# Optimization experiments

Measured on AMD Instinct MI355X. Metric: run time of the kernel, lower is better.

Reference implementation:

```python
import jax, jax.numpy as jnp
import numpy as np

B, N, N2 = 4, 4096, 4096
CIN, DIM, KNN, UP = 128, 64, 20, 2
HPOS, HATT = 64, 256
EPS = 1e-5


def _group(feat, idx):
    # feat: (B,C,M), idx: (B,N,K) -> (B,C,N,K) gather of neighbor features
    return jax.vmap(lambda f, i: f[:, i])(feat, idx)


def _conv1d(w, b, x):
    # 1x1 Conv1d: w (O,C), x (B,C,N)
    return jnp.einsum('oc,bcn->bon', w, x) + b[:, None]


def _bn(x, g, be, m, v):
    # eval-mode BatchNorm2d on (B,C,N,K)
    inv = g / jnp.sqrt(v + EPS)
    return x * inv[:, None, None] + (be - m * inv)[:, None, None]


def setup_inputs() -> dict:
    key = jax.random.key(0)
    ks = jax.random.split(key, 32)
    r = lambda i, s: jax.random.normal(ks[i], s, jnp.float32)
    u = lambda i, s: jax.random.uniform(ks[i], s, jnp.float32, 0.5, 1.5)
    return {
        'pos1': r(0, (B, 3, N)),
        'query': r(1, (B, CIN, N)),
        'pos2': r(2, (B, 3, N2)),
        'key_feat': r(3, (B, CIN, N2)),
        'wq': r(4, (DIM, CIN)) * 0.05, 'bq': r(5, (DIM,)) * 0.05,
        'wk': r(6, (DIM, CIN)) * 0.05, 'bk': r(7, (DIM,)) * 0.05,
        'wv': r(8, (DIM, CIN)) * 0.05, 'bv': r(9, (DIM,)) * 0.05,
        'pw1': r(10, (HPOS, 3)) * 0.2, 'pb1': r(11, (HPOS,)) * 0.05,
        'pg': u(12, (HPOS,)), 'pbt': r(13, (HPOS,)) * 0.05,
        'pm': r(14, (HPOS,)) * 0.05, 'pv': u(15, (HPOS,)),
        'pw2': r(16, (DIM, HPOS)) * 0.1, 'pb2': r(17, (DIM,)) * 0.05,
        'aw1': r(18, (HATT, DIM)) * 0.1, 'ab1': r(19, (HATT,)) * 0.05,
        'ag': u(20, (HATT,)), 'abt2': r(21, (HATT,)) * 0.05,
        'am': r(22, (HATT,)) * 0.05, 'av': u(23, (HATT,)),
        'awt': r(24, (HATT, DIM, UP)) * 0.05, 'abt': r(25, (DIM,)) * 0.05,
        'we': r(26, (CIN, DIM)) * 0.1, 'be': r(27, (CIN,)) * 0.05,
    }


def reference(pos1, query, pos2, key_feat, wq, bq, wk, bk, wv, bv,
              pw1, pb1, pg, pbt, pm, pv, pw2, pb2,
              aw1, ab1, ag, abt2, am, av, awt, abt, we, be):
    q = _conv1d(wq, bq, query)          # (B,DIM,N)
    k = _conv1d(wk, bk, key_feat)       # (B,DIM,N2)
    v = _conv1d(wv, bv, key_feat)       # (B,DIM,N2)
    # KNN of pos1 queries into pos2 support set
    p1 = pos1.transpose(0, 2, 1)        # (B,N,3)
    p2 = pos2.transpose(0, 2, 1)        # (B,N2,3)
    d = (jnp.sum(p1 * p1, -1)[:, :, None] + jnp.sum(p2 * p2, -1)[:, None, :]
         - 2.0 * jnp.einsum('bnd,bmd->bnm', p1, p2))
    _, idx = jax.lax.top_k(-d, KNN)     # (B,N,KNN)
    kg = _group(k, idx)                 # (B,DIM,N,K)
    qk_rel = q[:, :, :, None] - kg
    pos_rel = pos1[:, :, :, None] - _group(pos2, idx)   # (B,3,N,K)
    # pos_mlp: conv2d 3->HPOS, BN, ReLU, conv2d HPOS->DIM
    pe = jnp.einsum('oc,bcnk->bonk', pw1, pos_rel) + pb1[:, None, None]
    pe = jax.nn.relu(_bn(pe, pg, pbt, pm, pv))
    pe = jnp.einsum('oc,bcnk->bonk', pw2, pe) + pb2[:, None, None]  # (B,DIM,N,K)
    # attn_mlp: conv2d DIM->HATT, BN, ReLU, ConvTranspose2d HATT->DIM kernel (UP,1)
    h = qk_rel + pe
    a = jnp.einsum('oc,bcnk->bonk', aw1, h) + ab1[:, None, None]
    a = jax.nn.relu(_bn(a, ag, abt2, am, av))               # (B,HATT,N,K)
    att = jnp.einsum('bcnk,cor->bonrk', a, awt).reshape(B, DIM, N * UP, KNN)
    att = att + abt[:, None, None]
    att = jax.nn.softmax(att, axis=-1)
    vg = _group(v, idx) + pe            # (B,DIM,N,K)
    vu = jnp.repeat(vg, UP, axis=2)     # nearest upsample -> (B,DIM,N*UP,K)
    agg = jnp.sum(att * vu, axis=-1)    # (B,DIM,N*UP)
    y = _conv1d(we, be, agg)            # (B,CIN,N*UP)
    identity = jnp.repeat(query, UP, axis=2)  # residual (in==out -> Identity)
    return y + identity
```

## Files before the change

### kernel.cpp

```cpp
#include <hip/hip_runtime.h>
#include <hip/hip_bf16.h>

#define BATCH 4
#define NPTS  4096
#define NPTS2 4096
#define CIN   128
#define DIM   64
#define KNN   20
#define UPF   2
#define HPOS  64
#define HATT  256
#define MOUT  8192
#define EPSF  1e-5f
#define QPB   3
#define BPB   1366

typedef _Float16 h16x8 __attribute__((ext_vector_type(8)));
typedef _Float16 h16x4 __attribute__((ext_vector_type(4)));
typedef _Float16 h16x2 __attribute__((ext_vector_type(2)));
typedef float    f32x4 __attribute__((ext_vector_type(4)));

__device__ inline float rdlane(float v, int src) {
  return __int_as_float(__builtin_amdgcn_readlane(__float_as_int(v), src));
}

__device__ __forceinline__ float distf(float qn, float m2x, float m2y, float m2z,
                                       float x, float y, float z) {
  float s = __fmaf_rn(x, x, qn);
  s = __fmaf_rn(y, y, s);
  s = __fmaf_rn(z, z, s);
  s = __fmaf_rn(m2x, x, s);
  s = __fmaf_rn(m2y, y, s);
  s = __fmaf_rn(m2z, z, s);
  return s;
}

__global__ __launch_bounds__(256) void proj_q(const float* __restrict__ x,
    const float* __restrict__ wq, const float* __restrict__ bq,
    float* __restrict__ q_t) {
  __shared__ float X[CIN][64];
  __shared__ float O[64][65];
  const int b  = blockIdx.x >> 6;
  const int n0 = (blockIdx.x & 63) * 64;
  const int t  = threadIdx.x;
  for (int l = t; l < CIN * 64; l += 256) {
    int c = l >> 6, i = l & 63;
    X[c][i] = x[(b * CIN + c) * NPTS + n0 + i];
  }
  __syncthreads();
  const int n_l = t & 63;
  const int w   = __builtin_amdgcn_readfirstlane(t >> 6);
  float acc[16];
#pragma unroll
  for (int i = 0; i < 16; ++i) acc[i] = bq[w * 16 + i];
  for (int c = 0; c < CIN; ++c) {
    float xv = X[c][n_l];
#pragma unroll
    for (int i = 0; i < 16; ++i) acc[i] += wq[(w * 16 + i) * CIN + c] * xv;
  }
#pragma unroll
  for (int i = 0; i < 16; ++i) O[n_l][w * 16 + i] = acc[i];
  __syncthreads();
  for (int l = t; l < 64 * 64; l += 256)
    q_t[(b * NPTS + n0 + (l >> 6)) * DIM + (l & 63)] = O[l >> 6][l & 63];
}

__global__ __launch_bounds__(256) void proj_kv(const float* __restrict__ x,
    const float* __restrict__ wk, const float* __restrict__ bk,
    const float* __restrict__ wv, const float* __restrict__ bv,
    float* __restrict__ k_t, float* __restrict__ v_t) {
  __shared__ float X[CIN][64];
  __shared__ float O[64][65];
  const int b  = blockIdx.x >> 6;
  const int n0 = (blockIdx.x & 63) * 64;
  const int t  = threadIdx.x;
  for (int l = t; l < CIN * 64; l += 256) {
    int c = l >> 6, i = l & 63;
    X[c][i] = x[(b * CIN + c) * NPTS2 + n0 + i];
  }
  __syncthreads();
  const int n_l = t & 63;
  const int w   = __builtin_amdgcn_readfirstlane(t >> 6);
  float acck[16], accv[16];
#pragma unroll
  for (int i = 0; i < 16; ++i) { acck[i] = bk[w * 16 + i]; accv[i] = bv[w * 16 + i]; }
  for (int c = 0; c < CIN; ++c) {
    float xv = X[c][n_l];
#pragma unroll
    for (int i = 0; i < 16; ++i) {
      acck[i] += wk[(w * 16 + i) * CIN + c] * xv;
      accv[i] += wv[(w * 16 + i) * CIN + c] * xv;
    }
  }
#pragma unroll
  for (int i = 0; i < 16; ++i) O[n_l][w * 16 + i] = acck[i];
  __syncthreads();
  for (int l = t; l < 64 * 64; l += 256)
    k_t[(b * NPTS2 + n0 + (l >> 6)) * DIM + (l & 63)] = O[l >> 6][l & 63];
  __syncthreads();
#pragma unroll
  for (int i = 0; i < 16; ++i) O[n_l][w * 16 + i] = accv[i];
  __syncthreads();
  for (int l = t; l < 64 * 64; l += 256)
    v_t[(b * NPTS2 + n0 + (l >> 6)) * DIM + (l & 63)] = O[l >> 6][l & 63];
}

__global__ __launch_bounds__(256) void knn_kernel(const float* __restrict__ pos1,
    const float* __restrict__ pos2, int* __restrict__ idxout) {
  __shared__ int   cntS[4];
  __shared__ float dbufS[4][64];
  __shared__ int   jbufS[4][64];
  const int lane = threadIdx.x & 63;
  const int wv   = threadIdx.x >> 6;
  const int g    = blockIdx.x * 4 + wv;
  const int b    = g >> 12;
  const int n    = g & (NPTS - 1);
  const float qx = pos1[(b * 3 + 0) * NPTS + n];
  const float qy = pos1[(b * 3 + 1) * NPTS + n];
  const float qz = pos1[(b * 3 + 2) * NPTS + n];
  const float qn = qx * qx + qy * qy + qz * qz;
  const float m2x = -2.0f * qx, m2y = -2.0f * qy, m2z = -2.0f * qz;
  const float* p2x = pos2 + (b * 3 + 0) * NPTS2;
  const float* p2y = pos2 + (b * 3 + 1) * NPTS2;
  const float* p2z = pos2 + (b * 3 + 2) * NPTS2;

  float mymin = 3.402823466e38f;
  for (int j0 = 0; j0 < NPTS2; j0 += 64) {
    int j = j0 + lane;
    float d = distf(qn, m2x, m2y, m2z, p2x[j], p2y[j], p2z[j]);
    mymin = fminf(mymin, d);
  }
  float v = mymin;
#pragma unroll
  for (int k = 2; k <= 64; k <<= 1) {
#pragma unroll
    for (int jj = k >> 1; jj >= 1; jj >>= 1) {
      float o = __shfl_xor(v, jj);
      bool up = ((lane & k) == 0);
      bool keepmin = (((lane & jj) == 0) == up);
      v = keepmin ? fminf(v, o) : fmaxf(v, o);
    }
  }
  const float T0 = rdlane(v, 19);

  if (lane == 0) cntS[wv] = 0;
  __syncthreads();

  for (int j0 = 0; j0 < NPTS2; j0 += 64) {
    int j = j0 + lane;
    float d = distf(qn, m2x, m2y, m2z, p2x[j], p2y[j], p2z[j]);
    if (d <= T0) {
      int slot = atomicAdd(&cntS[wv], 1);
      if (slot < 64) { dbufS[wv][slot] = d; jbufS[wv][slot] = j; }
    }
  }
  __syncthreads();

  const int cnt = cntS[wv];
  if (cnt <= 64) {
    float dk = (lane < cnt) ? dbufS[wv][lane] : 3.402823466e38f;
    int   jk = (lane < cnt) ? jbufS[wv][lane] : 0x7fffffff;
#pragma unroll
    for (int k = 2; k <= 64; k <<= 1) {
#pragma unroll
      for (int jj = k >> 1; jj >= 1; jj >>= 1) {
        float od = __shfl_xor(dk, jj);
        int   oj = __shfl_xor(jk, jj);
        bool mineSm = (dk < od) || (dk == od && jk < oj);
        bool up = ((lane & k) == 0);
        bool keepmin = (((lane & jj) == 0) == up);
        bool takeOther = (keepmin != mineSm);
        dk = takeOther ? od : dk;
        jk = takeOther ? oj : jk;
      }
    }
    if (lane < KNN) idxout[(b * NPTS + n) * KNN + lane] = jk;
  } else {
    float dl = 3.402823466e38f;
    int   il = 0;
    for (int j0 = 0; j0 < NPTS2; j0 += 64) {
      int j = j0 + lane;
      float d = distf(qn, m2x, m2y, m2z, p2x[j], p2y[j], p2z[j]);
      float T = rdlane(dl, 19);
      unsigned long long m = __ballot(d < T);
      while (m) {
        int src = __ffsll(m) - 1;
        m &= m - 1;
        float dd = rdlane(d, src);
        float T2 = rdlane(dl, 19);
        if (dd < T2) {
          int jj2 = j0 + src;
          float pd = __shfl_up(dl, 1);
          int   pi = __shfl_up(il, 1);
          if (dl > dd) {
            if (lane == 0 || pd <= dd) { dl = dd; il = jj2; }
            else                       { dl = pd; il = pi; }
          }
        }
      }
    }
    if (lane < KNN) idxout[(b * NPTS + n) * KNN + lane] = il;
  }
}

__global__ __launch_bounds__(256) void pack_weights(
    const float* __restrict__ aw1, const float* __restrict__ awt,
    const float* __restrict__ pw2,
    const float* __restrict__ ag,  const float* __restrict__ av,
    const float* __restrict__ abt2, const float* __restrict__ am,
    const float* __restrict__ abt,
    const float* __restrict__ pg,  const float* __restrict__ pv,
    const float* __restrict__ pbt, const float* __restrict__ pm,
    const float* __restrict__ ab1, const float* __restrict__ pb1,
    const float* __restrict__ pw1,
    _Float16* __restrict__ aw1h, _Float16* __restrict__ awtP,
    _Float16* __restrict__ pw2h, float* __restrict__ abtX,
    float* __restrict__ ab1f, float* __restrict__ pw1f,
    float* __restrict__ pb1f) {
  int i = blockIdx.x * 256 + threadIdx.x;
  if (i < 16384) {
    int j = i >> 6;
    float inv = ag[j] / sqrtf(av[j] + EPSF);
    aw1h[i] = (_Float16)(aw1[i] * inv);
  }
  if (i < 32768) {
    int orr = i >> 8, j = i & 255;
    awtP[i] = (_Float16)awt[j * 128 + orr];
  }
  if (i < 4096) pw2h[i] = (_Float16)pw2[i];
  if (i < 256) {
    float inv = ag[i] / sqrtf(av[i] + EPSF);
    ab1f[i] = ab1[i] * inv + (abt2[i] - am[i] * inv);
  }
  if (i < 192) {
    int hc = i / 3;
    float inv = pg[hc] / sqrtf(pv[hc] + EPSF);
    pw1f[i] = pw1[i] * inv;
  }
  if (i < 128) abtX[i] = abt[i >> 1];
  if (i < 64) {
    float inv = pg[i] / sqrtf(pv[i] + EPSF);
    pb1f[i] = pb1[i] * inv + (pbt[i] - pm[i] * inv);
  }
}

#define SM_H1B   0
#define SM_HB    0
#define SM_ALQ   0
#define SM_PEL   9216
#define SM_LGC   9216
#define SM_SJ    17920
#define SM_VGB   18176

__global__ __launch_bounds__(256, 4) void attn_mfma(
    const float* __restrict__ q_t, const float* __restrict__ k_t,
    const float* __restrict__ v_t, const int* __restrict__ idx,
    const float* __restrict__ pos1, const float* __restrict__ pos2,
    const float* __restrict__ pw1f, const float* __restrict__ pb1f,
    const _Float16* __restrict__ pw2h, const float* __restrict__ pb2,
    const _Float16* __restrict__ aw1h, const float* __restrict__ ab1f,
    const _Float16* __restrict__ awtP, const float* __restrict__ abtX,
    float* __restrict__ agg) {
  __shared__ __align__(16) char smem[26880];
  const int b  = blockIdx.x / BPB;
  const int n0 = (blockIdx.x - b * BPB) * QPB;
  const int t  = threadIdx.x;
  const int lane = t & 63;
  const int w  = t >> 6;
  const int r  = lane & 15;
  const int q4 = lane >> 4;

  int* sj = (int*)(smem + SM_SJ);

  if (t < 64) {
    int col = t;
    int p = col / 20, kk = col - p * 20;
    int nq = n0 + p;
    int vI = 0;
    if (p < QPB && nq < NPTS) vI = idx[(b * NPTS + nq) * KNN + kk];
    sj[col] = vI;
  }
  __syncthreads();

  const int colB = t & 63, cgB = t >> 6;
  const int pB = colB / 20;
  const bool okB = (pB < QPB) && (n0 + pB < NPTS);
  f32x4 qv4[4], kv4[4], vv4[4];
  {
    int jB  = sj[colB];
    int nqB = okB ? (n0 + pB) : 0;
    const float* qrow = q_t + ((size_t)(b * NPTS  + nqB)) * DIM + cgB * 16;
    const float* krow = k_t + ((size_t)(b * NPTS2 + jB))  * DIM + cgB * 16;
    const float* vrow = v_t + ((size_t)(b * NPTS2 + jB))  * DIM + cgB * 16;
#pragma unroll
    for (int u = 0; u < 4; ++u) {
      qv4[u] = *(const f32x4*)(qrow + u * 4);
      kv4[u] = *(const f32x4*)(krow + u * 4);
      vv4[u] = *(const f32x4*)(vrow + u * 4);
    }
  }

  {
    int col = t & 63, hg = t >> 6;
    int p = col / 20;
    int j = sj[col];
    bool okc = (p < QPB) && (n0 + p < NPTS);
    float p0 = 0.f, p1 = 0.f, p2 = 0.f;
    if (okc) {
      int nq = n0 + p;
      p0 = pos1[(b * 3 + 0) * NPTS + nq] - pos2[(b * 3 + 0) * NPTS2 + j];
      p1 = pos1[(b * 3 + 1) * NPTS + nq] - pos2[(b * 3 + 1) * NPTS2 + j];
      p2 = pos1[(b * 3 + 2) * NPTS + nq] - pos2[(b * 3 + 2) * NPTS2 + j];
    }
#pragma unroll
    for (int ii = 0; ii < 16; ii += 2) {
      int hc = hg * 16 + ii;
      float v0 = pb1f[hc]     + pw1f[hc*3]   * p0 + pw1f[hc*3+1] * p1 + pw1f[hc*3+2] * p2;
      float v1 = pb1f[hc + 1] + pw1f[hc*3+3] * p0 + pw1f[hc*3+4] * p1 + pw1f[hc*3+5] * p2;
      v0 = fmaxf(v0, 0.f);
      v1 = fmaxf(v1, 0.f);
      if (!okc) { v0 = 0.f; v1 = 0.f; }
      h16x2 pk = {(_Float16)v0, (_Float16)v1};
      *(h16x2*)(smem + SM_H1B + ((col * 72 + hc) * 2)) = pk;
    }
  }
  __syncthreads();

  {
    h16x8 a0[2];
#pragma unroll
    for (int ks = 0; ks < 2; ++ks)
      a0[ks] = *(const h16x8*)&pw2h[(w * 16 + r) * 64 + ks * 32 + q4 * 8];
    f32x4 acc[4];
#pragma unroll
    for (int nt = 0; nt < 4; ++nt) acc[nt] = (f32x4){0.f, 0.f, 0.f, 0.f};
#pragma unroll
    for (int ks = 0; ks < 2; ++ks)
#pragma unroll
      for (int nt = 0; nt < 4; ++nt) {
        h16x8 bv = *(h16x8*)(smem + SM_H1B + ((nt * 16 + r) * 72 + ks * 32 + q4 * 8) * 2);
        acc[nt] = __builtin_amdgcn_mfma_f32_16x16x32_f16(a0[ks], bv, acc[nt], 0, 0, 0);
      }
    int o0 = w * 16 + q4 * 4;
    f32x4 pbv = *(const f32x4*)&pb2[o0];
#pragma unroll
    for (int nt = 0; nt < 4; ++nt) {
      f32x4 vv = acc[nt] + pbv;
      h16x4 pk = {(_Float16)vv[0], (_Float16)vv[1], (_Float16)vv[2], (_Float16)vv[3]};
      *(h16x4*)(smem + SM_PEL + ((nt * 16 + r) * 68 + o0) * 2) = pk;
    }
  }
  __syncthreads();

  {
#pragma unroll
    for (int u = 0; u < 4; ++u) {
      int c0 = cgB * 16 + u * 4;
      h16x4 peh = *(h16x4*)(smem + SM_PEL + (colB * 68 + c0) * 2);
      f32x4 pe = {(float)peh[0], (float)peh[1], (float)peh[2], (float)peh[3]};
      f32x4 hv = qv4[u] - kv4[u] + pe;
      f32x4 gv = vv4[u] + pe;
      if (!okB) { hv = (f32x4){0.f,0.f,0.f,0.f}; gv = hv; }
      h16x4 hp = {(_Float16)hv[0], (_Float16)hv[1], (_Float16)hv[2], (_Float16)hv[3]};
      h16x4 gp = {(_Float16)gv[0], (_Float16)gv[1], (_Float16)gv[2], (_Float16)gv[3]};
      *(h16x4*)(smem + SM_HB  + (colB * 72 + c0) * 2) = hp;
      *(h16x4*)(smem + SM_VGB + (colB * 68 + c0) * 2) = gp;
    }
  }
  __syncthreads();

  h16x8 bs[2][4];
#pragma unroll
  for (int ks = 0; ks < 2; ++ks)
#pragma unroll
    for (int nt = 0; nt < 4; ++nt)
      bs[ks][nt] = *(h16x8*)(smem + SM_HB + ((nt * 16 + r) * 72 + ks * 32 + q4 * 8) * 2);
  __syncthreads();

  f32x4 accD[2][4];
#pragma unroll
  for (int h = 0; h < 2; ++h)
#pragma unroll
    for (int nt = 0; nt < 4; ++nt) accD[h][nt] = (f32x4){0.f, 0.f, 0.f, 0.f};

#pragma unroll
  for (int quar = 0; quar < 4; ++quar) {
    {
      int mt = quar * 4 + w;
      h16x8 af0 = *(const h16x8*)&aw1h[(mt * 16 + r) * 64 + q4 * 8];
      h16x8 af1 = *(const h16x8*)&aw1h[(mt * 16 + r) * 64 + 32 + q4 * 8];
      f32x4 acc[4];
#pragma unroll
      for (int nt = 0; nt < 4; ++nt) acc[nt] = (f32x4){0.f, 0.f, 0.f, 0.f};
#pragma unroll
      for (int nt = 0; nt < 4; ++nt)
        acc[nt] = __builtin_amdgcn_mfma_f32_16x16x32_f16(af0, bs[0][nt], acc[nt], 0, 0, 0);
#pragma unroll
      for (int nt = 0; nt < 4; ++nt)
        acc[nt] = __builtin_amdgcn_mfma_f32_16x16x32_f16(af1, bs[1][nt], acc[nt], 0, 0, 0);
      int j0  = mt * 16 + q4 * 4;
      int jq0 = j0 - quar * 64;
      f32x4 b1 = *(const f32x4*)&ab1f[j0];
#pragma unroll
      for (int nt = 0; nt < 4; ++nt) {
        int col = nt * 16 + r;
        float v0 = fmaxf(acc[nt][0] + b1[0], 0.f);
        float v1 = fmaxf(acc[nt][1] + b1[1], 0.f);
        float v2 = fmaxf(acc[nt][2] + b1[2], 0.f);
        float v3 = fmaxf(acc[nt][3] + b1[3], 0.f);
        h16x4 pk = {(_Float16)v0, (_Float16)v1, (_Float16)v2, (_Float16)v3};
        *(h16x4*)(smem + SM_ALQ + (col * 72 + jq0) * 2) = pk;
      }
    }
    __syncthreads();

#pragma unroll
    for (int ks2 = 0; ks2 < 2; ++ks2) {
      h16x8 bsv[4];
#pragma unroll
      for (int nt = 0; nt < 4; ++nt)
        bsv[nt] = *(h16x8*)(smem + SM_ALQ + ((nt * 16 + r) * 72 + ks2 * 32 + q4 * 8) * 2);
      int ksg = quar * 2 + ks2;
#pragma unroll
      for (int h = 0; h < 2; ++h) {
        int mt2 = w * 2 + h;
        h16x8 af = *(const h16x8*)&awtP[(mt2 * 16 + r) * 256 + ksg * 32 + q4 * 8];
#pragma unroll
        for (int nt = 0; nt < 4; ++nt)
          accD[h][nt] = __builtin_amdgcn_mfma_f32_16x16x32_f16(af, bsv[nt], accD[h][nt], 0, 0, 0);
      }
    }
    __syncthreads();
  }

  {
    const int li0 = w * 16 + q4 * 4;
#pragma unroll
    for (int h = 0; h < 2; ++h) {
      if (h) __syncthreads();
      int orr0 = (w * 2 + h) * 16 + q4 * 4;
      f32x4 ab = *(const f32x4*)&abtX[orr0];
#pragma unroll
      for (int nt = 0; nt < 4; ++nt) {
        int col = nt * 16 + r;
        if (col < QPB * KNN) {
          f32x4 vv = accD[h][nt] + ab;
          h16x4 pk = {(_Float16)vv[0], (_Float16)vv[1], (_Float16)vv[2], (_Float16)vv[3]};
          *(h16x4*)(smem + SM_LGC + (col * 68 + li0) * 2) = pk;
        }
      }
      __syncthreads();
      if (t < 64 * QPB) {
        int li = t & 63, p = t >> 6;
        if (n0 + p < NPTS) {
          int w2 = li >> 4;
          int orr = w2 * 32 + h * 16 + (li & 15);
          int o = orr >> 1, rb = orr & 1;
          float L[KNN];
#pragma unroll
          for (int kk = 0; kk < KNN; ++kk)
            L[kk] = (float)*(_Float16*)(smem + SM_LGC + (((p * 20 + kk) * 68 + li) * 2));
          float mx = L[0];
#pragma unroll
          for (int kk = 1; kk < KNN; ++kk) mx = fmaxf(mx, L[kk]);
          float s = 0.f;
#pragma unroll
          for (int kk = 0; kk < KNN; ++kk) { L[kk] = __expf(L[kk] - mx); s += L[kk]; }
          float rs = 1.0f / s;
          float a = 0.f;
#pragma unroll
          for (int kk = 0; kk < KNN; ++kk) {
            _Float16 gv = *(_Float16*)(smem + SM_VGB + (((p * 20 + kk) * 68 + o) * 2));
            a += L[kk] * (float)gv;
          }
          agg[(((size_t)(b * NPTS + n0 + p)) * UPF + rb) * DIM + o] = a * rs;
        }
      }
    }
  }
}

__global__ __launch_bounds__(256) void out_proj(const float* __restrict__ agg,
    const float* __restrict__ we, const float* __restrict__ be,
    const float* __restrict__ query, float* __restrict__ out) {
  __shared__ float A[64][65];
  const int b  = blockIdx.x >> 7;
  const int m0 = (blockIdx.x & 127) * 64;
  const int t  = threadIdx.x;
  for (int l = t; l < 64 * 64; l += 256) {
    int row = l >> 6, c = l & 63;
    A[row][c] = agg[(b * MOUT + m0 + row) * DIM + c];
  }
  __syncthreads();
  const int m_l = t & 63;
  const int w   = __builtin_amdgcn_readfirstlane(t >> 6);
  float acc[32];
#pragma unroll
  for (int i = 0; i < 32; ++i) acc[i] = 0.f;
  for (int c = 0; c < DIM; ++c) {
    float a = A[m_l][c];
#pragma unroll
    for (int i = 0; i < 32; ++i) acc[i] += we[(w * 32 + i) * DIM + c] * a;
  }
  const int m = m0 + m_l;
#pragma unroll
  for (int i = 0; i < 32; ++i) {
    int o = w * 32 + i;
    out[(b * CIN + o) * MOUT + m] = acc[i] + be[o] + query[(b * CIN + o) * NPTS + (m >> 1)];
  }
}

extern "C" void kernel_launch(void* const* d_in, const int* in_sizes, int n_in,
                              void* d_out, int out_size, void* d_ws, size_t ws_size,
                              hipStream_t stream) {
  (void)in_sizes; (void)n_in; (void)out_size; (void)ws_size;
  const float* pos1     = (const float*)d_in[0];
  const float* query    = (const float*)d_in[1];
  const float* pos2     = (const float*)d_in[2];
  const float* key_feat = (const float*)d_in[3];
  const float* wq  = (const float*)d_in[4];
  const float* bq  = (const float*)d_in[5];
  const float* wk  = (const float*)d_in[6];
  const float* bk  = (const float*)d_in[7];
  const float* wv  = (const float*)d_in[8];
  const float* bv  = (const float*)d_in[9];
  const float* pw1 = (const float*)d_in[10];
  const float* pb1 = (const float*)d_in[11];
  const float* pg  = (const float*)d_in[12];
  const float* pbt = (const float*)d_in[13];
  const float* pm  = (const float*)d_in[14];
  const float* pv  = (const float*)d_in[15];
  const float* pw2 = (const float*)d_in[16];
  const float* pb2 = (const float*)d_in[17];
  const float* aw1 = (const float*)d_in[18];
  const float* ab1 = (const float*)d_in[19];
  const float* ag  = (const float*)d_in[20];
  const float* abt2= (const float*)d_in[21];
  const float* am  = (const float*)d_in[22];
  const float* av  = (const float*)d_in[23];
  const float* awt = (const float*)d_in[24];
  const float* abt = (const float*)d_in[25];
  const float* we  = (const float*)d_in[26];
  const float* be  = (const float*)d_in[27];

  float* ws   = (float*)d_ws;
  float* q_t  = ws;
  float* k_t  = q_t + BATCH * NPTS * DIM;
  float* v_t  = k_t + BATCH * NPTS2 * DIM;
  float* aggb = v_t + BATCH * NPTS2 * DIM;
  int*   idxb = (int*)(aggb + BATCH * MOUT * DIM);
  _Float16* aw1h = (_Float16*)(idxb + BATCH * NPTS * KNN);
  _Float16* awtP = aw1h + HATT * DIM;
  _Float16* pw2h = awtP + 128 * HATT;
  float* abtX    = (float*)(pw2h + DIM * HPOS);
  float* ab1f    = abtX + 128;
  float* pw1f    = ab1f + HATT;
  float* pb1f    = pw1f + HPOS * 3;

  pack_weights<<<128, 256, 0, stream>>>(aw1, awt, pw2, ag, av, abt2, am, abt,
      pg, pv, pbt, pm, ab1, pb1, pw1,
      aw1h, awtP, pw2h, abtX, ab1f, pw1f, pb1f);
  proj_q <<<BATCH * (NPTS / 64), 256, 0, stream>>>(query, wq, bq, q_t);
  proj_kv<<<BATCH * (NPTS2 / 64), 256, 0, stream>>>(key_feat, wk, bk, wv, bv, k_t, v_t);
  knn_kernel<<<BATCH * NPTS / 4, 256, 0, stream>>>(pos1, pos2, idxb);
  attn_mfma<<<BATCH * BPB, 256, 0, stream>>>(q_t, k_t, v_t, idxb, pos1, pos2,
      pw1f, pb1f, pw2h, pb2, aw1h, ab1f, awtP, abtX, aggb);
  out_proj<<<BATCH * (MOUT / 64), 256, 0, stream>>>(aggb, we, be, query, (float*)d_out);
}
```

Baseline: 384.5 us.

## Double-buffer attention LDS stages and cut barriers in attn_mfma

Reorganizes shared memory so the four hidden-dim quarter stages alternate between two buffers, which removes one block barrier per quarter. The neighbor index is now loaded directly per thread instead of being staged through LDS behind a barrier. A barrier that was only ordering same-wave accesses is dropped. All logits are written at once so softmax and aggregation run in a single pass instead of two barrier-separated halves. In exchange the kernel uses more LDS per block, which may limit occupancy, and correctness now depends on the chosen buffer offsets not overlapping between stages.

```diff
diff --git a/kernel.cpp b/kernel.cpp
--- a/kernel.cpp
+++ b/kernel.cpp
@@ -244,13 +244,11 @@
   }
 }
 
-#define SM_H1B   0
-#define SM_HB    0
-#define SM_ALQ   0
-#define SM_PEL   9216
-#define SM_LGC   9216
-#define SM_SJ    17920
-#define SM_VGB   18176
+#define SM_R0    0
+#define SM_R1    9216
+#define SM_BUF1  18432
+#define SM_LGC   0
+#define SM_VGB   27648
 
 __global__ __launch_bounds__(256, 4) void attn_mfma(
     const float* __restrict__ q_t, const float* __restrict__ k_t,
@@ -261,7 +259,7 @@
     const _Float16* __restrict__ aw1h, const float* __restrict__ ab1f,
     const _Float16* __restrict__ awtP, const float* __restrict__ abtX,
     float* __restrict__ agg) {
-  __shared__ __align__(16) char smem[26880];
+  __shared__ __align__(16) char smem[36352];
   const int b  = blockIdx.x / BPB;
   const int n0 = (blockIdx.x - b * BPB) * QPB;
   const int t  = threadIdx.x;
@@ -270,25 +268,15 @@
   const int r  = lane & 15;
   const int q4 = lane >> 4;
 
-  int* sj = (int*)(smem + SM_SJ);
-
-  if (t < 64) {
-    int col = t;
-    int p = col / 20, kk = col - p * 20;
-    int nq = n0 + p;
-    int vI = 0;
-    if (p < QPB && nq < NPTS) vI = idx[(b * NPTS + nq) * KNN + kk];
-    sj[col] = vI;
-  }
-  __syncthreads();
-
   const int colB = t & 63, cgB = t >> 6;
-  const int pB = colB / 20;
+  const int pB = colB / 20, kkB = colB - pB * 20;
   const bool okB = (pB < QPB) && (n0 + pB < NPTS);
+  const int nqB = okB ? (n0 + pB) : 0;
+  int jB = 0;
+  if (okB) jB = idx[(b * NPTS + nqB) * KNN + kkB];
+
   f32x4 qv4[4], kv4[4], vv4[4];
   {
-    int jB  = sj[colB];
-    int nqB = okB ? (n0 + pB) : 0;
     const float* qrow = q_t + ((size_t)(b * NPTS  + nqB)) * DIM + cgB * 16;
     const float* krow = k_t + ((size_t)(b * NPTS2 + jB))  * DIM + cgB * 16;
     const float* vrow = v_t + ((size_t)(b * NPTS2 + jB))  * DIM + cgB * 16;
@@ -301,27 +289,22 @@
   }
 
   {
-    int col = t & 63, hg = t >> 6;
-    int p = col / 20;
-    int j = sj[col];
-    bool okc = (p < QPB) && (n0 + p < NPTS);
     float p0 = 0.f, p1 = 0.f, p2 = 0.f;
-    if (okc) {
-      int nq = n0 + p;
-      p0 = pos1[(b * 3 + 0) * NPTS + nq] - pos2[(b * 3 + 0) * NPTS2 + j];
-      p1 = pos1[(b * 3 + 1) * NPTS + nq] - pos2[(b * 3 + 1) * NPTS2 + j];
-      p2 = pos1[(b * 3 + 2) * NPTS + nq] - pos2[(b * 3 + 2) * NPTS2 + j];
+    if (okB) {
+      p0 = pos1[(b * 3 + 0) * NPTS + nqB] - pos2[(b * 3 + 0) * NPTS2 + jB];
+      p1 = pos1[(b * 3 + 1) * NPTS + nqB] - pos2[(b * 3 + 1) * NPTS2 + jB];
+      p2 = pos1[(b * 3 + 2) * NPTS + nqB] - pos2[(b * 3 + 2) * NPTS2 + jB];
     }
 #pragma unroll
     for (int ii = 0; ii < 16; ii += 2) {
-      int hc = hg * 16 + ii;
+      int hc = cgB * 16 + ii;
       float v0 = pb1f[hc]     + pw1f[hc*3]   * p0 + pw1f[hc*3+1] * p1 + pw1f[hc*3+2] * p2;
       float v1 = pb1f[hc + 1] + pw1f[hc*3+3] * p0 + pw1f[hc*3+4] * p1 + pw1f[hc*3+5] * p2;
       v0 = fmaxf(v0, 0.f);
       v1 = fmaxf(v1, 0.f);
-      if (!okc) { v0 = 0.f; v1 = 0.f; }
+      if (!okB) { v0 = 0.f; v1 = 0.f; }
       h16x2 pk = {(_Float16)v0, (_Float16)v1};
-      *(h16x2*)(smem + SM_H1B + ((col * 72 + hc) * 2)) = pk;
+      *(h16x2*)(smem + SM_R0 + ((colB * 72 + hc) * 2)) = pk;
     }
   }
   __syncthreads();
@@ -338,7 +321,7 @@
     for (int ks = 0; ks < 2; ++ks)
 #pragma unroll
       for (int nt = 0; nt < 4; ++nt) {
-        h16x8 bv = *(h16x8*)(smem + SM_H1B + ((nt * 16 + r) * 72 + ks * 32 + q4 * 8) * 2);
+        h16x8 bv = *(h16x8*)(smem + SM_R0 + ((nt * 16 + r) * 72 + ks * 32 + q4 * 8) * 2);
         acc[nt] = __builtin_amdgcn_mfma_f32_16x16x32_f16(a0[ks], bv, acc[nt], 0, 0, 0);
       }
     int o0 = w * 16 + q4 * 4;
@@ -347,23 +330,22 @@
     for (int nt = 0; nt < 4; ++nt) {
       f32x4 vv = acc[nt] + pbv;
       h16x4 pk = {(_Float16)vv[0], (_Float16)vv[1], (_Float16)vv[2], (_Float16)vv[3]};
-      *(h16x4*)(smem + SM_PEL + ((nt * 16 + r) * 68 + o0) * 2) = pk;
-    }
-  }
-  __syncthreads();
+      *(h16x4*)(smem + SM_R1 + ((nt * 16 + r) * 72 + o0) * 2) = pk;
+    }
+  }
 
   {
 #pragma unroll
     for (int u = 0; u < 4; ++u) {
       int c0 = cgB * 16 + u * 4;
-      h16x4 peh = *(h16x4*)(smem + SM_PEL + (colB * 68 + c0) * 2);
+      h16x4 peh = *(h16x4*)(smem + SM_R1 + (colB * 72 + c0) * 2);
       f32x4 pe = {(float)peh[0], (float)peh[1], (float)peh[2], (float)peh[3]};
       f32x4 hv = qv4[u] - kv4[u] + pe;
       f32x4 gv = vv4[u] + pe;
       if (!okB) { hv = (f32x4){0.f,0.f,0.f,0.f}; gv = hv; }
       h16x4 hp = {(_Float16)hv[0], (_Float16)hv[1], (_Float16)hv[2], (_Float16)hv[3]};
       h16x4 gp = {(_Float16)gv[0], (_Float16)gv[1], (_Float16)gv[2], (_Float16)gv[3]};
-      *(h16x4*)(smem + SM_HB  + (colB * 72 + c0) * 2) = hp;
+      *(h16x4*)(smem + SM_R1  + (colB * 72 + c0) * 2) = hp;
       *(h16x4*)(smem + SM_VGB + (colB * 68 + c0) * 2) = gp;
     }
   }
@@ -374,8 +356,7 @@
   for (int ks = 0; ks < 2; ++ks)
 #pragma unroll
     for (int nt = 0; nt < 4; ++nt)
-      bs[ks][nt] = *(h16x8*)(smem + SM_HB + ((nt * 16 + r) * 72 + ks * 32 + q4 * 8) * 2);
-  __syncthreads();
+      bs[ks][nt] = *(h16x8*)(smem + SM_R1 + ((nt * 16 + r) * 72 + ks * 32 + q4 * 8) * 2);
 
   f32x4 accD[2][4];
 #pragma unroll
@@ -383,61 +364,71 @@
 #pragma unroll
     for (int nt = 0; nt < 4; ++nt) accD[h][nt] = (f32x4){0.f, 0.f, 0.f, 0.f};
 
-#pragma unroll
-  for (int quar = 0; quar < 4; ++quar) {
-    {
-      int mt = quar * 4 + w;
-      h16x8 af0 = *(const h16x8*)&aw1h[(mt * 16 + r) * 64 + q4 * 8];
-      h16x8 af1 = *(const h16x8*)&aw1h[(mt * 16 + r) * 64 + 32 + q4 * 8];
-      f32x4 acc[4];
-#pragma unroll
-      for (int nt = 0; nt < 4; ++nt) acc[nt] = (f32x4){0.f, 0.f, 0.f, 0.f};
-#pragma unroll
-      for (int nt = 0; nt < 4; ++nt)
-        acc[nt] = __builtin_amdgcn_mfma_f32_16x16x32_f16(af0, bs[0][nt], acc[nt], 0, 0, 0);
-#pragma unroll
-      for (int nt = 0; nt < 4; ++nt)
-        acc[nt] = __builtin_amdgcn_mfma_f32_16x16x32_f16(af1, bs[1][nt], acc[nt], 0, 0, 0);
-      int j0  = mt * 16 + q4 * 4;
-      int jq0 = j0 - quar * 64;
-      f32x4 b1 = *(const f32x4*)&ab1f[j0];
-#pragma unroll
-      for (int nt = 0; nt < 4; ++nt) {
-        int col = nt * 16 + r;
-        float v0 = fmaxf(acc[nt][0] + b1[0], 0.f);
-        float v1 = fmaxf(acc[nt][1] + b1[1], 0.f);
-        float v2 = fmaxf(acc[nt][2] + b1[2], 0.f);
-        float v3 = fmaxf(acc[nt][3] + b1[3], 0.f);
-        h16x4 pk = {(_Float16)v0, (_Float16)v1, (_Float16)v2, (_Float16)v3};
-        *(h16x4*)(smem + SM_ALQ + (col * 72 + jq0) * 2) = pk;
-      }
-    }
-    __syncthreads();
-
-#pragma unroll
-    for (int ks2 = 0; ks2 < 2; ++ks2) {
-      h16x8 bsv[4];
-#pragma unroll
-      for (int nt = 0; nt < 4; ++nt)
-        bsv[nt] = *(h16x8*)(smem + SM_ALQ + ((nt * 16 + r) * 72 + ks2 * 32 + q4 * 8) * 2);
-      int ksg = quar * 2 + ks2;
-#pragma unroll
-      for (int h = 0; h < 2; ++h) {
-        int mt2 = w * 2 + h;
-        h16x8 af = *(const h16x8*)&awtP[(mt2 * 16 + r) * 256 + ksg * 32 + q4 * 8];
-#pragma unroll
-        for (int nt = 0; nt < 4; ++nt)
-          accD[h][nt] = __builtin_amdgcn_mfma_f32_16x16x32_f16(af, bsv[nt], accD[h][nt], 0, 0, 0);
-      }
-    }
-    __syncthreads();
-  }
+#define C_QUARTER(quar, base)                                                  \
+  {                                                                            \
+    int mt = (quar) * 4 + w;                                                   \
+    h16x8 af0 = *(const h16x8*)&aw1h[(mt * 16 + r) * 64 + q4 * 8];             \
+    h16x8 af1 = *(const h16x8*)&aw1h[(mt * 16 + r) * 64 + 32 + q4 * 8];        \
+    f32x4 acc[4];                                                              \
+    _Pragma("unroll")                                                          \
+    for (int nt = 0; nt < 4; ++nt) acc[nt] = (f32x4){0.f, 0.f, 0.f, 0.f};      \
+    _Pragma("unroll")                                                          \
+    for (int nt = 0; nt < 4; ++nt)                                             \
+      acc[nt] = __builtin_amdgcn_mfma_f32_16x16x32_f16(af0, bs[0][nt], acc[nt], 0, 0, 0); \
+    _Pragma("unroll")                                                          \
+    for (int nt = 0; nt < 4; ++nt)                                             \
+      acc[nt] = __builtin_amdgcn_mfma_f32_16x16x32_f16(af1, bs[1][nt], acc[nt], 0, 0, 0); \
+    int j0  = mt * 16 + q4 * 4;                                                \
+    int jq0 = j0 - (quar) * 64;                                                \
+    f32x4 b1 = *(const f32x4*)&ab1f[j0];                                       \
+    _Pragma("unroll")                                                          \
+    for (int nt = 0; nt < 4; ++nt) {                                           \
+      int col = nt * 16 + r;                                                   \
+      float v0 = fmaxf(acc[nt][0] + b1[0], 0.f);                               \
+      float v1 = fmaxf(acc[nt][1] + b1[1], 0.f);                               \
+      float v2 = fmaxf(acc[nt][2] + b1[2], 0.f);                               \
+      float v3 = fmaxf(acc[nt][3] + b1[3], 0.f);                               \
+      h16x4 pk = {(_Float16)v0, (_Float16)v1, (_Float16)v2, (_Float16)v3};     \
+      *(h16x4*)(smem + (base) + (col * 72 + jq0) * 2) = pk;                    \
+    }                                                                          \
+  }
+
+#define D_QUARTER(quar, base)                                                  \
+  {                                                                            \
+    _Pragma("unroll")                                                          \
+    for (int ks2 = 0; ks2 < 2; ++ks2) {                                        \
+      h16x8 bsv[4];                                                            \
+      _Pragma("unroll")                                                        \
+      for (int nt = 0; nt < 4; ++nt)                                           \
+        bsv[nt] = *(h16x8*)(smem + (base) + ((nt * 16 + r) * 72 + ks2 * 32 + q4 * 8) * 2); \
+      int ksg = (quar) * 2 + ks2;                                              \
+      _Pragma("unroll")                                                        \
+      for (int h = 0; h < 2; ++h) {                                            \
+        int mt2 = w * 2 + h;                                                   \
+        h16x8 af = *(const h16x8*)&awtP[(mt2 * 16 + r) * 256 + ksg * 32 + q4 * 8]; \
+        _Pragma("unroll")                                                      \
+        for (int nt = 0; nt < 4; ++nt)                                         \
+          accD[h][nt] = __builtin_amdgcn_mfma_f32_16x16x32_f16(af, bsv[nt], accD[h][nt], 0, 0, 0); \
+      }                                                                        \
+    }                                                                          \
+  }
+
+  C_QUARTER(0, SM_R0)
+  __syncthreads();
+  D_QUARTER(0, SM_R0)
+  C_QUARTER(1, SM_BUF1)
+  __syncthreads();
+  D_QUARTER(1, SM_BUF1)
+  C_QUARTER(2, SM_R0)
+  __syncthreads();
+  D_QUARTER(2, SM_R0)
+  C_QUARTER(3, SM_BUF1)
+  __syncthreads();
+  D_QUARTER(3, SM_BUF1)
 
   {
-    const int li0 = w * 16 + q4 * 4;
 #pragma unroll
     for (int h = 0; h < 2; ++h) {
-      if (h) __syncthreads();
       int orr0 = (w * 2 + h) * 16 + q4 * 4;
       f32x4 ab = *(const f32x4*)&abtX[orr0];
 #pragma unroll
@@ -446,38 +437,43 @@
         if (col < QPB * KNN) {
           f32x4 vv = accD[h][nt] + ab;
           h16x4 pk = {(_Float16)vv[0], (_Float16)vv[1], (_Float16)vv[2], (_Float16)vv[3]};
-          *(h16x4*)(smem + SM_LGC + (col * 68 + li0) * 2) = pk;
+          *(h16x4*)(smem + SM_LGC + (col * 136 + orr0) * 2) = pk;
         }
       }
-      __syncthreads();
-      if (t < 64 * QPB) {
-        int li = t & 63, p = t >> 6;
-        if (n0 + p < NPTS) {
-          int w2 = li >> 4;
-          int orr = w2 * 32 + h * 16 + (li & 15);
-          int o = orr >> 1, rb = orr & 1;
-          float L[KNN];
-#pragma unroll
-          for (int kk = 0; kk < KNN; ++kk)
-            L[kk] = (float)*(_Float16*)(smem + SM_LGC + (((p * 20 + kk) * 68 + li) * 2));
-          float mx = L[0];
-#pragma unroll
-          for (int kk = 1; kk < KNN; ++kk) mx = fmaxf(mx, L[kk]);
-          float s = 0.f;
-#pragma unroll
-          for (int kk = 0; kk < KNN; ++kk) { L[kk] = __expf(L[kk] - mx); s += L[kk]; }
-          float rs = 1.0f / s;
-          float a = 0.f;
-#pragma unroll
-          for (int kk = 0; kk < KNN; ++kk) {
-            _Float16 gv = *(_Float16*)(smem + SM_VGB + (((p * 20 + kk) * 68 + o) * 2));
-            a += L[kk] * (float)gv;
-          }
-          agg[(((size_t)(b * NPTS + n0 + p)) * UPF + rb) * DIM + o] = a * rs;
+    }
+  }
+  __syncthreads();
+
+  if (t < 64 * QPB) {
+    int li = t & 63, p = t >> 6;
+    if (n0 + p < NPTS) {
+#pragma unroll
+      for (int half = 0; half < 2; ++half) {
+        int orr = (li >> 4) * 32 + half * 16 + (li & 15);
+        int o = orr >> 1, rb = orr & 1;
+        float L[KNN];
+#pragma unroll
+        for (int kk = 0; kk < KNN; ++kk)
+          L[kk] = (float)*(_Float16*)(smem + SM_LGC + (((p * 20 + kk) * 136 + orr) * 2));
+        float mx = L[0];
+#pragma unroll
+        for (int kk = 1; kk < KNN; ++kk) mx = fmaxf(mx, L[kk]);
+        float s = 0.f;
+#pragma unroll
+        for (int kk = 0; kk < KNN; ++kk) { L[kk] = __expf(L[kk] - mx); s += L[kk]; }
+        float rs = 1.0f / s;
+        float a = 0.f;
+#pragma unroll
+        for (int kk = 0; kk < KNN; ++kk) {
+          _Float16 gv = *(_Float16*)(smem + SM_VGB + (((p * 20 + kk) * 68 + o) * 2));
+          a += L[kk] * (float)gv;
         }
+        agg[(((size_t)(b * NPTS + n0 + p)) * UPF + rb) * DIM + o] = a * rs;
       }
     }
   }
+#undef C_QUARTER
+#undef D_QUARTER
 }
 
 __global__ __launch_bounds__(256) void out_proj(const float* __restrict__ agg,
```

Measured after the change: 381.9 us. About the same (-0.7%).
